# Kernel tuning notes

Measured on AMD Instinct MI355X. Metric: run time of the kernel, lower is better.

Reference implementation:

```python
import jax, jax.numpy as jnp
import numpy as np

B, S, I, H, HI = 1024, 64, 2048, 2048, 2048  # batch, num_high_states, input_dim, hidden_dim, high_dim
L = 4          # num recurrent layers
NH = 16        # num heads
HD = H // NH   # head dim
MAX_STEPS = 100


def setup_inputs() -> dict:
    key = jax.random.key(0)
    ks = iter(jax.random.split(key, 40))
    std = 0.02
    d = {}
    d["x"] = jax.random.normal(next(ks), (B, I), jnp.float32)
    d["high_state"] = jax.random.normal(next(ks), (B, HI), jnp.float32)
    d["high_states_history"] = jax.random.normal(next(ks), (B, S, HI), jnp.float32)
    d["hidden"] = jax.random.normal(next(ks), (L, B, H), jnp.float32) * 0.1
    # input projection + timestep embedding
    d["W_in"] = jax.random.normal(next(ks), (I, H), jnp.float32) * std
    d["b_in"] = jnp.zeros((H,), jnp.float32)
    d["ts_emb"] = jax.random.normal(next(ks), (MAX_STEPS, H), jnp.float32) * std
    # hierarchical attention projections
    d["Wq"] = jax.random.normal(next(ks), (H, H), jnp.float32) * std
    d["bq"] = jnp.zeros((H,), jnp.float32)
    d["Wk"] = jax.random.normal(next(ks), (HI, H), jnp.float32) * std
    d["bk"] = jnp.zeros((H,), jnp.float32)
    d["Wv"] = jax.random.normal(next(ks), (HI, H), jnp.float32) * std
    d["bv"] = jnp.zeros((H,), jnp.float32)
    d["Wo"] = jax.random.normal(next(ks), (H, H), jnp.float32) * std
    d["bo"] = jnp.zeros((H,), jnp.float32)
    # per-layer GRU-like gates, stacked over layers; Linear in = I+H = 2H
    for nm in ("Wu", "Wr", "Ws", "Wc"):
        d[nm] = jax.random.normal(next(ks), (L, 2 * H, H), jnp.float32) * std
    for nm in ("bu", "br", "bs", "bc"):
        d[nm] = jnp.zeros((L, H), jnp.float32)
    # layer norm
    d["ln_g"] = jnp.ones((H,), jnp.float32)
    d["ln_b"] = jnp.zeros((H,), jnp.float32)
    d["timestep"] = 5
    return d


def _forward(x, high_states_history, hidden, W_in, b_in, ts_emb,
             Wq, bq, Wk, bk, Wv, bv, Wo, bo,
             Wu, bu, Wr, br, Ws, bs, Wc, bc, ln_g, ln_b, timestep):
    # input projection + timestep encoding
    x = x @ W_in + b_in + ts_emb[timestep]  # [B,H]
    # hierarchical attention (single query per batch element)
    q = (x @ Wq + bq).reshape(B, NH, HD)
    k = (high_states_history @ Wk + bk).reshape(B, S, NH, HD)
    v = (high_states_history @ Wv + bv).reshape(B, S, NH, HD)
    scores = jnp.einsum("bhd,bshd->bhs", q, k) / np.sqrt(HD).astype(np.float32)
    attn = jax.nn.softmax(scores, axis=-1)  # [B,NH,S]
    ctx = jnp.einsum("bhs,bshd->bhd", attn, v).reshape(B, H)
    x = x + (ctx @ Wo + bo)
    # stacked GRU-like recurrent layers (loop over fixed small L)
    new_hidden = []
    for i in range(L):
        h = hidden[i]
        comb = jnp.concatenate([x, h], axis=1)  # [B,2H]
        u = jax.nn.sigmoid(comb @ Wu[i] + bu[i])
        r = jax.nn.sigmoid(comb @ Wr[i] + br[i])
        s = jax.nn.sigmoid(comb @ Ws[i] + bs[i])
        comb_r = jnp.concatenate([x, r * h], axis=1)
        cand = jax.nn.gelu(comb_r @ Wc[i] + bc[i], approximate=False)
        new_h = (1 - u) * h + u * (s * cand + (1 - s) * h)
        new_hidden.append(new_h)
        x = new_h  # dropout is identity in eval
    # layer norm (eps matches torch default 1e-5)
    mu = jnp.mean(x, axis=-1, keepdims=True)
    var = jnp.mean(jnp.square(x - mu), axis=-1, keepdims=True)
    out = (x - mu) * jax.lax.rsqrt(var + 1e-5) * ln_g + ln_b
    return out, jnp.stack(new_hidden)


def reference(x, high_state, high_states_history, hidden, W_in, b_in, ts_emb,
              Wq, bq, Wk, bk, Wv, bv, Wo, bo,
              Wu, bu, Wr, br, Ws, bs, Wc, bc, ln_g, ln_b, timestep):
    # high_state is accepted by the original signature but unused in the body
    return _forward(x, high_states_history, hidden, W_in, b_in, ts_emb,
                    Wq, bq, Wk, bk, Wv, bv, Wo, bo,
                    Wu, bu, Wr, br, Ws, bs, Wc, bc, ln_g, ln_b, timestep)
```

## Files before the change

kernel.cpp:

```cpp
#include <hip/hip_runtime.h>
#include <hip/hip_bf16.h>
#include <math.h>

#define B_  1024
#define S_  64
#define H_  2048
#define L_  4
#define NH_ 16
#define HD_ 128
#define WSLAB_ ((size_t)2048 * 4096)

typedef __attribute__((ext_vector_type(4))) float floatx4;
typedef __attribute__((ext_vector_type(8))) short shortx8;

__device__ __forceinline__ unsigned short f2bf(float f) {
  union { float f; unsigned int u; } v; v.f = f;
  unsigned int u = v.u;
  return (unsigned short)((u + 0x7fffu + ((u >> 16) & 1u)) >> 16);
}

__device__ __forceinline__ void gload16(const void* g, void* l) {
  __builtin_amdgcn_global_load_lds(
      (const __attribute__((address_space(1))) void*)g,
      (__attribute__((address_space(3))) void*)l, 16, 0, 0);
}

__global__ __launch_bounds__(256) void cvt_bf(
    const float* __restrict__ in, unsigned short* __restrict__ out, int n8)
{
  int i = blockIdx.x * 256 + threadIdx.x;
  if (i >= n8) return;
  const float4* p = (const float4*)in;
  float4 a = p[i * 2], b = p[i * 2 + 1];
  unsigned short o[8] = { f2bf(a.x), f2bf(a.y), f2bf(a.z), f2bf(a.w),
                          f2bf(b.x), f2bf(b.y), f2bf(b.z), f2bf(b.w) };
  ((uint4*)out)[i] = *(uint4*)o;
}

__global__ __launch_bounds__(256) void tconv4(
    const float* __restrict__ s0, const float* __restrict__ s1,
    const float* __restrict__ s2, const float* __restrict__ s3,
    unsigned short* __restrict__ dst, int K)
{
  const float* src = (blockIdx.z == 0) ? s0 : (blockIdx.z == 1) ? s1
                   : (blockIdx.z == 2) ? s2 : s3;
  unsigned short* out = dst + (size_t)blockIdx.z * 2048 * K;
  __shared__ float tile[64][65];
  int k0 = blockIdx.x * 64, n0 = blockIdx.y * 64;
  int t = threadIdx.x;
  int tr = t >> 4, tc = (t & 15) * 4;
  #pragma unroll
  for (int rep = 0; rep < 4; ++rep) {
    int kk = tr + rep * 16;
    float4 v = *(const float4*)(src + (size_t)(k0 + kk) * 2048 + n0 + tc);
    tile[kk][tc] = v.x; tile[kk][tc + 1] = v.y;
    tile[kk][tc + 2] = v.z; tile[kk][tc + 3] = v.w;
  }
  __syncthreads();
  int nr = t >> 2, kc = (t & 3) * 16;
  unsigned short o[16];
  #pragma unroll
  for (int j = 0; j < 16; ++j) o[j] = f2bf(tile[kc + j][nr]);
  *(uint4*)(out + (size_t)(n0 + nr) * K + k0 + kc)     = *(uint4*)&o[0];
  *(uint4*)(out + (size_t)(n0 + nr) * K + k0 + kc + 8) = *(uint4*)&o[8];
}

enum { EPI_XIN = 0, EPI_QB = 1, EPI_X2 = 2 };

template<int EPI, int MF, int NZ>
__global__ __launch_bounds__(256) void gemm128(
    int K,
    const unsigned short* __restrict__ A0,
    const unsigned short* __restrict__ BT,
    const float* __restrict__ b0,
    const float* __restrict__ tse, const int* __restrict__ tsp,
    const float* __restrict__ res,
    float* __restrict__ Cf, unsigned short* __restrict__ Cb)
{
  constexpr int BM = MF * 32;
  constexpr int NPAN = 16 * NZ;
  const int t = threadIdx.x, wid = t >> 6, lane = t & 63, lr = lane & 15, lg = lane >> 4;
  const int wr = wid >> 1, wc = wid & 1;
  const int g = blockIdx.x;
  const int m_base = (g / NPAN) * BM;
  const int pan = g % NPAN;
  const int n_base = (pan & 15) * 128;
  __shared__ unsigned short lds_a[BM * 32];
  __shared__ unsigned short lds_b[128 * 32];
  floatx4 acc[MF][4] = {};
  const int nkt = K >> 5;
  for (int kt = 0; kt < nkt; ++kt) {
    #pragma unroll
    for (int is = 0; is < BM / 64; ++is) {
      int idx = is * 256 + t;
      int row = idx >> 2, kc = idx & 3;
      int kcs = kc ^ ((row >> 1) & 3);
      int gk = kt * 32 + kcs * 8;
      gload16(A0 + (size_t)(m_base + row) * K + gk, &lds_a[(is * 256 + wid * 64) * 8]);
    }
    #pragma unroll
    for (int is = 0; is < 2; ++is) {
      int idx = is * 256 + t;
      int row = idx >> 2, kc = idx & 3;
      int kcs = kc ^ ((row >> 1) & 3);
      int gk = kt * 32 + kcs * 8;
      gload16(BT + (size_t)(n_base + row) * K + gk, &lds_b[(is * 256 + wid * 64) * 8]);
    }
    __syncthreads();
    const int sl = lg ^ ((lr >> 1) & 3);
    shortx8 af[MF], bfv[4];
    #pragma unroll
    for (int mt = 0; mt < MF; ++mt)
      af[mt] = *(shortx8*)&lds_a[(wr * (MF * 16) + mt * 16 + lr) * 32 + sl * 8];
    #pragma unroll
    for (int nt = 0; nt < 4; ++nt)
      bfv[nt] = *(shortx8*)&lds_b[(wc * 64 + nt * 16 + lr) * 32 + sl * 8];
    #pragma unroll
    for (int mt = 0; mt < MF; ++mt)
      #pragma unroll
      for (int nt = 0; nt < 4; ++nt)
        acc[mt][nt] = __builtin_amdgcn_mfma_f32_16x16x32_bf16(af[mt], bfv[nt], acc[mt][nt], 0, 0, 0);
    __syncthreads();
  }
  int ts = 0;
  if (EPI == EPI_XIN) ts = tsp[0];
  #pragma unroll
  for (int mt = 0; mt < MF; ++mt)
  #pragma unroll
  for (int nt = 0; nt < 4; ++nt)
  #pragma unroll
  for (int j = 0; j < 4; ++j) {
    int row = m_base + wr * (MF * 16) + mt * 16 + lg * 4 + j;
    int col = n_base + wc * 64 + nt * 16 + lr;
    size_t idx = (size_t)row * 2048 + col;
    float v = acc[mt][nt][j] + b0[col];
    if (EPI == EPI_XIN) {
      v += tse[(size_t)ts * 2048 + col];
      Cf[idx] = v; Cb[idx] = f2bf(v);
    } else if (EPI == EPI_QB) {
      Cb[idx] = f2bf(v);
    } else {
      v += res[idx]; Cb[idx] = f2bf(v);
    }
  }
}

__global__ __launch_bounds__(256, 4) void gemm_gates(
    const unsigned short* __restrict__ Ax, const unsigned short* __restrict__ Ah,
    const unsigned short* __restrict__ TW,
    const float* __restrict__ bu, const float* __restrict__ br, const float* __restrict__ bs,
    const float* __restrict__ Hf,
    float* __restrict__ U, float* __restrict__ Sg,
    unsigned short* __restrict__ rh, float* __restrict__ Cc)
{
  const int t = threadIdx.x, wid = t >> 6, lane = t & 63, lr = lane & 15, lg = lane >> 4;
  const int wr = wid >> 1, wc = wid & 1;
  const int g = blockIdx.x;
  const int m_base = (g >> 6) * 64;
  const int pan = g & 63;
  const int n_base = (pan & 15) * 128;
  const int z = pan >> 4;
  const unsigned short* BTz = TW + (size_t)z * WSLAB_;
  __shared__ unsigned short lds_a[64 * 32];
  __shared__ unsigned short lds_b[128 * 32];
  floatx4 acc[2][4] = {};
  const int nkt = (z == 3) ? 64 : 128;
  const int arow = t >> 2, akc = t & 3;
  const int akcs = akc ^ ((arow >> 1) & 3);
  for (int kt = 0; kt < nkt; ++kt) {
    {
      int gk = kt * 32 + akcs * 8;
      const unsigned short* ga;
      if (z == 3)           ga = Ax + (size_t)(m_base + arow) * 2048 + gk;
      else if (gk < 2048)   ga = Ax + (size_t)(m_base + arow) * 2048 + gk;
      else                  ga = Ah + (size_t)(m_base + arow) * 2048 + (gk - 2048);
      gload16(ga, &lds_a[wid * 512]);
    }
    #pragma unroll
    for (int is = 0; is < 2; ++is) {
      int idx = is * 256 + t;
      int row = idx >> 2, kc = idx & 3;
      int kcs = kc ^ ((row >> 1) & 3);
      int gk = kt * 32 + kcs * 8;
      gload16(BTz + (size_t)(n_base + row) * 4096 + gk, &lds_b[(is * 256 + wid * 64) * 8]);
    }
    __syncthreads();
    const int sl = lg ^ ((lr >> 1) & 3);
    shortx8 af[2], bfv[4];
    #pragma unroll
    for (int mt = 0; mt < 2; ++mt)
      af[mt] = *(shortx8*)&lds_a[(wr * 32 + mt * 16 + lr) * 32 + sl * 8];
    #pragma unroll
    for (int nt = 0; nt < 4; ++nt)
      bfv[nt] = *(shortx8*)&lds_b[(wc * 64 + nt * 16 + lr) * 32 + sl * 8];
    #pragma unroll
    for (int mt = 0; mt < 2; ++mt)
      #pragma unroll
      for (int nt = 0; nt < 4; ++nt)
        acc[mt][nt] = __builtin_amdgcn_mfma_f32_16x16x32_bf16(af[mt], bfv[nt], acc[mt][nt], 0, 0, 0);
    __syncthreads();
  }
  #pragma unroll
  for (int mt = 0; mt < 2; ++mt)
  #pragma unroll
  for (int nt = 0; nt < 4; ++nt)
  #pragma unroll
  for (int j = 0; j < 4; ++j) {
    int row = m_base + wr * 32 + mt * 16 + lg * 4 + j;
    int col = n_base + wc * 64 + nt * 16 + lr;
    size_t idx = (size_t)row * 2048 + col;
    float v = acc[mt][nt][j];
    if (z == 0)      U[idx]  = 1.f / (1.f + expf(-(v + bu[col])));
    else if (z == 1) rh[idx] = f2bf((1.f / (1.f + expf(-(v + br[col])))) * Hf[idx]);
    else if (z == 2) Sg[idx] = 1.f / (1.f + expf(-(v + bs[col])));
    else             Cc[idx] = v;
  }
}

__global__ __launch_bounds__(256, 4) void gemm_cand(
    const unsigned short* __restrict__ Arh, const unsigned short* __restrict__ TW,
    const float* __restrict__ bc, const float* __restrict__ Cc,
    const float* __restrict__ U, const float* __restrict__ Sg,
    const float* __restrict__ Hf,
    float* __restrict__ nh_f, unsigned short* __restrict__ nh_b)
{
  const int t = threadIdx.x, wid = t >> 6, lane = t & 63, lr = lane & 15, lg = lane >> 4;
  const int wr = wid >> 1, wc = wid & 1;
  const int g = blockIdx.x;
  const int m_base = (g >> 4) * 64;
  const int n_base = (g & 15) * 128;
  const unsigned short* BTz = TW + (size_t)3 * WSLAB_;
  __shared__ unsigned short lds_a[64 * 32];
  __shared__ unsigned short lds_b[128 * 32];
  floatx4 acc[2][4] = {};
  const int arow = t >> 2, akc = t & 3;
  const int akcs = akc ^ ((arow >> 1) & 3);
  for (int kt = 0; kt < 64; ++kt) {
    gload16(Arh + (size_t)(m_base + arow) * 2048 + kt * 32 + akcs * 8, &lds_a[wid * 512]);
    #pragma unroll
    for (int is = 0; is < 2; ++is) {
      int idx = is * 256 + t;
      int row = idx >> 2, kc = idx & 3;
      int kcs = kc ^ ((row >> 1) & 3);
      int gk = kt * 32 + kcs * 8;
      gload16(BTz + (size_t)(n_base + row) * 4096 + 2048 + gk, &lds_b[(is * 256 + wid * 64) * 8]);
    }
    __syncthreads();
    const int sl = lg ^ ((lr >> 1) & 3);
    shortx8 af[2], bfv[4];
    #pragma unroll
    for (int mt = 0; mt < 2; ++mt)
      af[mt] = *(shortx8*)&lds_a[(wr * 32 + mt * 16 + lr) * 32 + sl * 8];
    #pragma unroll
    for (int nt = 0; nt < 4; ++nt)
      bfv[nt] = *(shortx8*)&lds_b[(wc * 64 + nt * 16 + lr) * 32 + sl * 8];
    #pragma unroll
    for (int mt = 0; mt < 2; ++mt)
      #pragma unroll
      for (int nt = 0; nt < 4; ++nt)
        acc[mt][nt] = __builtin_amdgcn_mfma_f32_16x16x32_bf16(af[mt], bfv[nt], acc[mt][nt], 0, 0, 0);
    __syncthreads();
  }
  #pragma unroll
  for (int mt = 0; mt < 2; ++mt)
  #pragma unroll
  for (int nt = 0; nt < 4; ++nt)
  #pragma unroll
  for (int j = 0; j < 4; ++j) {
    int row = m_base + wr * 32 + mt * 16 + lg * 4 + j;
    int col = n_base + wc * 64 + nt * 16 + lr;
    size_t idx = (size_t)row * 2048 + col;
    float v = acc[mt][nt][j] + Cc[idx] + bc[col];
    float gl = 0.5f * v * (1.f + erff(v * 0.70710678118654752f));
    float u = U[idx], s = Sg[idx], hh = Hf[idx];
    float nh = (1.f - u) * hh + u * (s * gl + (1.f - s) * hh);
    nh_f[idx] = nh; nh_b[idx] = f2bf(nh);
  }
}

__global__ __launch_bounds__(256) void gemm_t(
    const unsigned short* __restrict__ Q, const unsigned short* __restrict__ Wk,
    unsigned short* __restrict__ T)
{
  const int t = threadIdx.x, wid = t >> 6, lane = t & 63, lr = lane & 15, lg = lane >> 4;
  const int wr = wid >> 1, wc = wid & 1;
  const int h = blockIdx.z, m_base = blockIdx.x * 64, n_base = blockIdx.y * 128;
  __shared__ unsigned short lds_a[64 * 32], lds_b[128 * 32];
  floatx4 acc[2][4] = {};
  const int arow = t >> 2, akc = t & 3;
  const int akcs = akc ^ ((arow >> 1) & 3);
  for (int kt = 0; kt < 4; ++kt) {
    gload16(Q + (size_t)(m_base + arow) * 2048 + h * 128 + kt * 32 + akcs * 8,
            &lds_a[wid * 512]);
    #pragma unroll
    for (int is = 0; is < 2; ++is) {
      int idx = is * 256 + t;
      int row = idx >> 2, kc = idx & 3;
      int kcs = kc ^ ((row >> 1) & 3);
      gload16(Wk + (size_t)(n_base + row) * 2048 + h * 128 + kt * 32 + kcs * 8,
              &lds_b[(is * 256 + wid * 64) * 8]);
    }
    __syncthreads();
    const int sl = lg ^ ((lr >> 1) & 3);
    shortx8 af[2], bfv[4];
    #pragma unroll
    for (int mt = 0; mt < 2; ++mt)
      af[mt] = *(shortx8*)&lds_a[(wr * 32 + mt * 16 + lr) * 32 + sl * 8];
    #pragma unroll
    for (int nt = 0; nt < 4; ++nt)
      bfv[nt] = *(shortx8*)&lds_b[(wc * 64 + nt * 16 + lr) * 32 + sl * 8];
    #pragma unroll
    for (int mt = 0; mt < 2; ++mt)
      #pragma unroll
      for (int nt = 0; nt < 4; ++nt)
        acc[mt][nt] = __builtin_amdgcn_mfma_f32_16x16x32_bf16(af[mt], bfv[nt], acc[mt][nt], 0, 0, 0);
    __syncthreads();
  }
  #pragma unroll
  for (int mt = 0; mt < 2; ++mt)
  #pragma unroll
  for (int nt = 0; nt < 4; ++nt)
  #pragma unroll
  for (int j = 0; j < 4; ++j) {
    int row_o = m_base + wr * 32 + mt * 16 + lg * 4 + j;
    int col   = n_base + wc * 64 + nt * 16 + lr;
    T[((size_t)row_o * 16 + h) * 2048 + col] = f2bf(acc[mt][nt][j]);
  }
}

__global__ __launch_bounds__(256) void attn_fused(
    const unsigned short* __restrict__ T, const float* __restrict__ hist,
    unsigned short* __restrict__ Wb)
{
  const int t = threadIdx.x;
  const int wid = t >> 6, lane = t & 63, lr = lane & 15, lg = lane >> 4;
  const int b = blockIdx.x;
  __shared__ unsigned short lds_t[16 * 72];
  __shared__ unsigned short lds_h[64 * 72];
  __shared__ float sc[16 * 68];
  __shared__ float ps[64 * 16];
  floatx4 acc = {};
  for (int kt = 0; kt < 32; ++kt) {
    { int row = t >> 4, c4 = t & 15;
      int k = kt * 64 + c4 * 4;
      ushort4 v = *(const ushort4*)(T + ((size_t)b * 16 + row) * 2048 + k);
      *(ushort4*)&lds_t[row * 72 + c4 * 4] = v; }
    #pragma unroll
    for (int rep = 0; rep < 4; ++rep) {
      int idx = t + rep * 256;
      int srow = idx >> 4, c4 = idx & 15;
      int k = kt * 64 + c4 * 4;
      float4 hv = *(const float4*)(hist + ((size_t)b * 64 + srow) * 2048 + k);
      ushort4 uv; uv.x = f2bf(hv.x); uv.y = f2bf(hv.y); uv.z = f2bf(hv.z); uv.w = f2bf(hv.w);
      *(ushort4*)&lds_h[srow * 72 + c4 * 4] = uv;
    }
    __syncthreads();
    #pragma unroll
    for (int ks = 0; ks < 2; ++ks) {
      shortx8 af = *(shortx8*)&lds_t[lr * 72 + ks * 32 + lg * 8];
      shortx8 bv = *(shortx8*)&lds_h[(wid * 16 + lr) * 72 + ks * 32 + lg * 8];
      acc = __builtin_amdgcn_mfma_f32_16x16x32_bf16(af, bv, acc, 0, 0, 0);
    }
    __syncthreads();
  }
  #pragma unroll
  for (int j = 0; j < 4; ++j)
    sc[(lg * 4 + j) * 68 + wid * 16 + lr] = acc[j] * 0.088388347648318447f;
  __syncthreads();
  if (t < 64) {
    int h = t >> 2, qd = t & 3;
    float vv[16];
    float m = -1e30f;
    #pragma unroll
    for (int zz = 0; zz < 16; ++zz) { vv[zz] = sc[h * 68 + qd * 16 + zz]; m = fmaxf(m, vv[zz]); }
    m = fmaxf(m, __shfl_xor(m, 1)); m = fmaxf(m, __shfl_xor(m, 2));
    float sum = 0.f;
    #pragma unroll
    for (int zz = 0; zz < 16; ++zz) { vv[zz] = expf(vv[zz] - m); sum += vv[zz]; }
    sum += __shfl_xor(sum, 1); sum += __shfl_xor(sum, 2);
    float inv = 1.f / sum;
    #pragma unroll
    for (int zz = 0; zz < 16; ++zz)
      ps[(qd * 16 + zz) * 16 + h] = vv[zz] * inv;
  }
  __syncthreads();
  const int i0 = t * 8;
  floatx4 wacc[16][2] = {};
  const floatx4* ps4 = (const floatx4*)ps;
  for (int s = 0; s < 64; ++s) {
    const float* hp = hist + ((size_t)b * 64 + s) * 2048 + i0;
    float4 h4a = *(const float4*)hp;
    float4 h4b = *(const float4*)(hp + 4);
    floatx4 hva = { h4a.x, h4a.y, h4a.z, h4a.w };
    floatx4 hvb = { h4b.x, h4b.y, h4b.z, h4b.w };
    #pragma unroll
    for (int hq = 0; hq < 4; ++hq) {
      floatx4 p = ps4[s * 4 + hq];
      wacc[hq * 4 + 0][0] += p.x * hva; wacc[hq * 4 + 0][1] += p.x * hvb;
      wacc[hq * 4 + 1][0] += p.y * hva; wacc[hq * 4 + 1][1] += p.y * hvb;
      wacc[hq * 4 + 2][0] += p.z * hva; wacc[hq * 4 + 2][1] += p.z * hvb;
      wacc[hq * 4 + 3][0] += p.w * hva; wacc[hq * 4 + 3][1] += p.w * hvb;
    }
  }
  #pragma unroll
  for (int h = 0; h < 16; ++h) {
    unsigned short o[8];
    #pragma unroll
    for (int j = 0; j < 4; ++j) { o[j] = f2bf(wacc[h][0][j]); o[4 + j] = f2bf(wacc[h][1][j]); }
    *(uint4*)(Wb + ((size_t)b * 16 + h) * 2048 + i0) = *(uint4*)o;
  }
}

__global__ __launch_bounds__(256) void gemm_ctx(
    const unsigned short* __restrict__ Wb, const unsigned short* __restrict__ WvT,
    const float* __restrict__ bv, unsigned short* __restrict__ ctx)
{
  const int t = threadIdx.x, wid = t >> 6, lane = t & 63, lr = lane & 15, lg = lane >> 4;
  const int wr = wid >> 1, wc = wid & 1;
  const int h = blockIdx.z, m_base = blockIdx.x * 64;
  __shared__ unsigned short lds_a[64 * 32], lds_b[128 * 32];
  floatx4 acc[2][4] = {};
  const int row = t >> 2, kc = t & 3;
  const int kcs = kc ^ ((row >> 1) & 3);
  for (int kt = 0; kt < 64; ++kt) {
    int gk = kt * 32 + kcs * 8;
    gload16(Wb  + ((size_t)(m_base + row) * 16 + h) * 2048 + gk, &lds_a[wid * 512]);
    gload16(WvT + (size_t)(h * 128 + row) * 2048 + gk,           &lds_b[wid * 512]);
    gload16(WvT + (size_t)(h * 128 + 64 + row) * 2048 + gk,      &lds_b[2048 + wid * 512]);
    __syncthreads();
    const int sl = lg ^ ((lr >> 1) & 3);
    shortx8 af[2], bfv[4];
    #pragma unroll
    for (int mt = 0; mt < 2; ++mt)
      af[mt] = *(shortx8*)&lds_a[(wr * 32 + mt * 16 + lr) * 32 + sl * 8];
    #pragma unroll
    for (int nt = 0; nt < 4; ++nt)
      bfv[nt] = *(shortx8*)&lds_b[(wc * 64 + nt * 16 + lr) * 32 + sl * 8];
    #pragma unroll
    for (int mt = 0; mt < 2; ++mt)
      #pragma unroll
      for (int nt = 0; nt < 4; ++nt)
        acc[mt][nt] = __builtin_amdgcn_mfma_f32_16x16x32_bf16(af[mt], bfv[nt], acc[mt][nt], 0, 0, 0);
    __syncthreads();
  }
  #pragma unroll
  for (int mt = 0; mt < 2; ++mt)
  #pragma unroll
  for (int nt = 0; nt < 4; ++nt)
  #pragma unroll
  for (int j = 0; j < 4; ++j) {
    int row_o = m_base + wr * 32 + mt * 16 + lg * 4 + j;
    int cl = wc * 64 + nt * 16 + lr;
    int gcol = h * 128 + cl;
    ctx[(size_t)row_o * 2048 + gcol] = f2bf(acc[mt][nt][j] + bv[gcol]);
  }
}

__global__ __launch_bounds__(256) void lnorm(
    const float* __restrict__ X, const float* __restrict__ gma,
    const float* __restrict__ bta, float* __restrict__ out)
{
  const int row = blockIdx.x, t = threadIdx.x;
  float4 a = *(const float4*)(X + (size_t)row * 2048 + t * 4);
  float4 c = *(const float4*)(X + (size_t)row * 2048 + 1024 + t * 4);
  float sum = a.x + a.y + a.z + a.w + c.x + c.y + c.z + c.w;
  float sq = a.x*a.x + a.y*a.y + a.z*a.z + a.w*a.w + c.x*c.x + c.y*c.y + c.z*c.z + c.w*c.w;
  #pragma unroll
  for (int off = 1; off < 64; off <<= 1) {
    sum += __shfl_xor(sum, off);
    sq  += __shfl_xor(sq, off);
  }
  __shared__ float red[8];
  int wid = t >> 6, lane = t & 63;
  if (lane == 0) { red[wid] = sum; red[wid + 4] = sq; }
  __syncthreads();
  sum = red[0] + red[1] + red[2] + red[3];
  sq  = red[4] + red[5] + red[6] + red[7];
  float mu = sum * (1.f / 2048.f);
  float var = sq * (1.f / 2048.f) - mu * mu;
  float rs = rsqrtf(var + 1e-5f);
  const float* pa = &a.x; const float* pc = &c.x;
  #pragma unroll
  for (int j = 0; j < 4; ++j) {
    int col = t * 4 + j;
    out[(size_t)row * 2048 + col] = (pa[j] - mu) * rs * gma[col] + bta[col];
  }
  #pragma unroll
  for (int j = 0; j < 4; ++j) {
    int col = 1024 + t * 4 + j;
    out[(size_t)row * 2048 + col] = (pc[j] - mu) * rs * gma[col] + bta[col];
  }
}

extern "C" void kernel_launch(void* const* d_in, const int* in_sizes, int n_in,
                              void* d_out, int out_size, void* d_ws, size_t ws_size,
                              hipStream_t stream) {
  (void)in_sizes; (void)n_in; (void)out_size; (void)ws_size;
  const float* x      = (const float*)d_in[0];
  const float* hist   = (const float*)d_in[2];
  const float* hidden = (const float*)d_in[3];
  const float* W_in   = (const float*)d_in[4];
  const float* b_in   = (const float*)d_in[5];
  const float* ts_emb = (const float*)d_in[6];
  const float* Wq     = (const float*)d_in[7];
  const float* bq     = (const float*)d_in[8];
  const float* Wk     = (const float*)d_in[9];
  const float* Wv     = (const float*)d_in[11];
  const float* bv     = (const float*)d_in[12];
  const float* Wo     = (const float*)d_in[13];
  const float* bo     = (const float*)d_in[14];
  const float* Wu     = (const float*)d_in[15];
  const float* Wr     = (const float*)d_in[16];
  const float* Wsg    = (const float*)d_in[17];
  const float* Wc     = (const float*)d_in[18];
  const float* bu     = (const float*)d_in[19];
  const float* br     = (const float*)d_in[20];
  const float* bs     = (const float*)d_in[21];
  const float* bc     = (const float*)d_in[22];
  const float* ln_g   = (const float*)d_in[23];
  const float* ln_b   = (const float*)d_in[24];
  const int*   tsp    = (const int*)d_in[25];
  float* out = (float*)d_out;

  const size_t BH = (size_t)B_ * H_;
  char* w = (char*)d_ws;
  auto take = [&](size_t bytes) { char* p = w; w += bytes; return p; };

  unsigned short* TW   = (unsigned short*)take((size_t)4 * WSLAB_ * 2);
  unsigned short* Tb   = (unsigned short*)take((size_t)B_ * 16 * 2048 * 2);
  unsigned short* WT4  = (unsigned short*)take((size_t)4 * H_ * H_ * 2);
  unsigned short* WinT = WT4;
  unsigned short* WqT  = WT4 + (size_t)H_ * H_;
  unsigned short* WvT  = WT4 + (size_t)2 * H_ * H_;
  unsigned short* WoT  = WT4 + (size_t)3 * H_ * H_;
  unsigned short* Wkb  = (unsigned short*)take((size_t)H_ * H_ * 2);
  unsigned short* x_bf   = (unsigned short*)take(BH * 2);
  unsigned short* h_bf   = (unsigned short*)take((size_t)L_ * BH * 2);
  unsigned short* xin_bf = (unsigned short*)take(BH * 2);
  unsigned short* q_bf   = (unsigned short*)take(BH * 2);
  unsigned short* ctx_bf = (unsigned short*)take(BH * 2);
  unsigned short* x2_bf  = (unsigned short*)take(BH * 2);
  unsigned short* rh_bf  = (unsigned short*)take(BH * 2);
  unsigned short* xa     = (unsigned short*)take(BH * 2);
  unsigned short* xb     = (unsigned short*)take(BH * 2);
  float* U   = (float*)take(BH * 4);
  float* Sg  = (float*)take(BH * 4);
  float* Cc  = (float*)take(BH * 4);
  float* XIN = out;

  dim3 blk(256);

  cvt_bf<<<dim3(1024), blk, 0, stream>>>(x, x_bf, (int)(BH / 8));
  cvt_bf<<<dim3(4096), blk, 0, stream>>>(hidden, h_bf, (int)(L_ * BH / 8));
  cvt_bf<<<dim3(2048), blk, 0, stream>>>(Wk, Wkb, (int)((size_t)H_ * H_ / 8));
  tconv4<<<dim3(32, 32, 4), blk, 0, stream>>>(W_in, Wq, Wv, Wo, WT4, 2048);

  gemm128<EPI_XIN, 2, 1><<<dim3(256), blk, 0, stream>>>(
      2048, x_bf, WinT, b_in, ts_emb, tsp, nullptr, XIN, xin_bf);
  gemm128<EPI_QB, 2, 1><<<dim3(256), blk, 0, stream>>>(
      2048, xin_bf, WqT, bq, nullptr, nullptr, nullptr, nullptr, q_bf);
  gemm_t<<<dim3(16, 16, 16), blk, 0, stream>>>(q_bf, Wkb, Tb);
  attn_fused<<<dim3(1024), blk, 0, stream>>>(Tb, hist, Tb);
  gemm_ctx<<<dim3(16, 1, 16), blk, 0, stream>>>(Tb, WvT, bv, ctx_bf);
  gemm128<EPI_X2, 2, 1><<<dim3(256), blk, 0, stream>>>(
      2048, ctx_bf, WoT, bo, nullptr, nullptr, XIN, nullptr, x2_bf);

  unsigned short* xcur = x2_bf;
  for (int i = 0; i < L_; ++i) {
    const float* h_i = hidden + (size_t)i * BH;
    float* nh_f = out + BH + (size_t)i * BH;
    unsigned short* nh_b = (i & 1) ? xb : xa;
    tconv4<<<dim3(64, 32, 4), blk, 0, stream>>>(
        Wu + (size_t)i * WSLAB_, Wr + (size_t)i * WSLAB_,
        Wsg + (size_t)i * WSLAB_, Wc + (size_t)i * WSLAB_, TW, 4096);
    gemm_gates<<<dim3(1024), blk, 0, stream>>>(
        xcur, h_bf + (size_t)i * BH, TW,
        bu + (size_t)i * H_, br + (size_t)i * H_, bs + (size_t)i * H_,
        h_i, U, Sg, rh_bf, Cc);
    gemm_cand<<<dim3(256), blk, 0, stream>>>(
        rh_bf, TW, bc + (size_t)i * H_, Cc, U, Sg, h_i, nh_f, nh_b);
    xcur = nh_b;
  }

  lnorm<<<dim3(1024), blk, 0, stream>>>(out + BH + (size_t)3 * BH, ln_g, ln_b, out);
}
```

Baseline: 1.262 ms.

## Overlap next-layer weight transpose with candidate GEMM via double-buffered slabs

Merges the next layer's fp32-to-bf16 weight transpose into the candidate GEMM launch as extra blocks. Two weight slabs are used as a double buffer so the conversion for layer i+1 runs alongside the 256-block cand GEMM for layer i, which on its own underfills the GPU. Layer 0's slab is converted up front. The cost is an extra 64MB workspace buffer and no longer forcing launch_bounds occupancy 4 on the GEMM blocks, which may change register allocation.

After: 1.250 ms. No clear change (-1.0%).

```diff
diff --git a/kernel.cpp b/kernel.cpp
--- a/kernel.cpp
+++ b/kernel.cpp
@@ -217,64 +217,96 @@
   }
 }
 
-__global__ __launch_bounds__(256, 4) void gemm_cand(
+__global__ __launch_bounds__(256) void cand_tconv(
     const unsigned short* __restrict__ Arh, const unsigned short* __restrict__ TW,
     const float* __restrict__ bc, const float* __restrict__ Cc,
     const float* __restrict__ U, const float* __restrict__ Sg,
     const float* __restrict__ Hf,
-    float* __restrict__ nh_f, unsigned short* __restrict__ nh_b)
-{
-  const int t = threadIdx.x, wid = t >> 6, lane = t & 63, lr = lane & 15, lg = lane >> 4;
-  const int wr = wid >> 1, wc = wid & 1;
-  const int g = blockIdx.x;
-  const int m_base = (g >> 4) * 64;
-  const int n_base = (g & 15) * 128;
-  const unsigned short* BTz = TW + (size_t)3 * WSLAB_;
-  __shared__ unsigned short lds_a[64 * 32];
-  __shared__ unsigned short lds_b[128 * 32];
-  floatx4 acc[2][4] = {};
-  const int arow = t >> 2, akc = t & 3;
-  const int akcs = akc ^ ((arow >> 1) & 3);
-  for (int kt = 0; kt < 64; ++kt) {
-    gload16(Arh + (size_t)(m_base + arow) * 2048 + kt * 32 + akcs * 8, &lds_a[wid * 512]);
-    #pragma unroll
-    for (int is = 0; is < 2; ++is) {
-      int idx = is * 256 + t;
-      int row = idx >> 2, kc = idx & 3;
-      int kcs = kc ^ ((row >> 1) & 3);
-      int gk = kt * 32 + kcs * 8;
-      gload16(BTz + (size_t)(n_base + row) * 4096 + 2048 + gk, &lds_b[(is * 256 + wid * 64) * 8]);
-    }
-    __syncthreads();
-    const int sl = lg ^ ((lr >> 1) & 3);
-    shortx8 af[2], bfv[4];
+    float* __restrict__ nh_f, unsigned short* __restrict__ nh_b,
+    const float* __restrict__ Wun, const float* __restrict__ Wrn,
+    const float* __restrict__ Wsn, const float* __restrict__ Wcn,
+    unsigned short* __restrict__ TWnext)
+{
+  __shared__ __align__(16) float smem[4224];
+  const int t = threadIdx.x;
+  if (blockIdx.x < 256) {
+    unsigned short* lds_a = (unsigned short*)smem;
+    unsigned short* lds_b = (unsigned short*)smem + 2048;
+    const int wid = t >> 6, lane = t & 63, lr = lane & 15, lg = lane >> 4;
+    const int wr = wid >> 1, wc = wid & 1;
+    const int g = blockIdx.x;
+    const int m_base = (g >> 4) * 64;
+    const int n_base = (g & 15) * 128;
+    const unsigned short* BTz = TW + (size_t)3 * WSLAB_;
+    floatx4 acc[2][4] = {};
+    const int arow = t >> 2, akc = t & 3;
+    const int akcs = akc ^ ((arow >> 1) & 3);
+    for (int kt = 0; kt < 64; ++kt) {
+      gload16(Arh + (size_t)(m_base + arow) * 2048 + kt * 32 + akcs * 8, &lds_a[wid * 512]);
+      #pragma unroll
+      for (int is = 0; is < 2; ++is) {
+        int idx = is * 256 + t;
+        int row = idx >> 2, kc = idx & 3;
+        int kcs = kc ^ ((row >> 1) & 3);
+        int gk = kt * 32 + kcs * 8;
+        gload16(BTz + (size_t)(n_base + row) * 4096 + 2048 + gk, &lds_b[(is * 256 + wid * 64) * 8]);
+      }
+      __syncthreads();
+      const int sl = lg ^ ((lr >> 1) & 3);
+      shortx8 af[2], bfv[4];
+      #pragma unroll
+      for (int mt = 0; mt < 2; ++mt)
+        af[mt] = *(shortx8*)&lds_a[(wr * 32 + mt * 16 + lr) * 32 + sl * 8];
+      #pragma unroll
+      for (int nt = 0; nt < 4; ++nt)
+        bfv[nt] = *(shortx8*)&lds_b[(wc * 64 + nt * 16 + lr) * 32 + sl * 8];
+      #pragma unroll
+      for (int mt = 0; mt < 2; ++mt)
+        #pragma unroll
+        for (int nt = 0; nt < 4; ++nt)
+          acc[mt][nt] = __builtin_amdgcn_mfma_f32_16x16x32_bf16(af[mt], bfv[nt], acc[mt][nt], 0, 0, 0);
+      __syncthreads();
+    }
     #pragma unroll
     for (int mt = 0; mt < 2; ++mt)
-      af[mt] = *(shortx8*)&lds_a[(wr * 32 + mt * 16 + lr) * 32 + sl * 8];
     #pragma unroll
     for (int nt = 0; nt < 4; ++nt)
-      bfv[nt] = *(shortx8*)&lds_b[(wc * 64 + nt * 16 + lr) * 32 + sl * 8];
-    #pragma unroll
-    for (int mt = 0; mt < 2; ++mt)
-      #pragma unroll
-      for (int nt = 0; nt < 4; ++nt)
-        acc[mt][nt] = __builtin_amdgcn_mfma_f32_16x16x32_bf16(af[mt], bfv[nt], acc[mt][nt], 0, 0, 0);
-    __syncthreads();
-  }
-  #pragma unroll
-  for (int mt = 0; mt < 2; ++mt)
-  #pragma unroll
-  for (int nt = 0; nt < 4; ++nt)
-  #pragma unroll
-  for (int j = 0; j < 4; ++j) {
-    int row = m_base + wr * 32 + mt * 16 + lg * 4 + j;
-    int col = n_base + wc * 64 + nt * 16 + lr;
-    size_t idx = (size_t)row * 2048 + col;
-    float v = acc[mt][nt][j] + Cc[idx] + bc[col];
-    float gl = 0.5f * v * (1.f + erff(v * 0.70710678118654752f));
-    float u = U[idx], s = Sg[idx], hh = Hf[idx];
-    float nh = (1.f - u) * hh + u * (s * gl + (1.f - s) * hh);
-    nh_f[idx] = nh; nh_b[idx] = f2bf(nh);
+    #pragma unroll
+    for (int j = 0; j < 4; ++j) {
+      int row = m_base + wr * 32 + mt * 16 + lg * 4 + j;
+      int col = n_base + wc * 64 + nt * 16 + lr;
+      size_t idx = (size_t)row * 2048 + col;
+      float v = acc[mt][nt][j] + Cc[idx] + bc[col];
+      float gl = 0.5f * v * (1.f + erff(v * 0.70710678118654752f));
+      float u = U[idx], s = Sg[idx], hh = Hf[idx];
+      float nh = (1.f - u) * hh + u * (s * gl + (1.f - s) * hh);
+      nh_f[idx] = nh; nh_b[idx] = f2bf(nh);
+    }
+  } else {
+    if (TWnext == nullptr) return;
+    float (*tile)[65] = (float(*)[65])smem;
+    int bid = blockIdx.x - 256;
+    int z = bid >> 11;
+    int rem = bid & 2047;
+    int k0 = (rem >> 5) * 64;
+    int n0 = (rem & 31) * 64;
+    const float* src = (z == 0) ? Wun : (z == 1) ? Wrn : (z == 2) ? Wsn : Wcn;
+    unsigned short* outp = TWnext + (size_t)z * WSLAB_;
+    int tr = t >> 4, tc = (t & 15) * 4;
+    #pragma unroll
+    for (int rep = 0; rep < 4; ++rep) {
+      int kk = tr + rep * 16;
+      float4 v = *(const float4*)(src + (size_t)(k0 + kk) * 2048 + n0 + tc);
+      tile[kk][tc] = v.x; tile[kk][tc + 1] = v.y;
+      tile[kk][tc + 2] = v.z; tile[kk][tc + 3] = v.w;
+    }
+    __syncthreads();
+    int nr = t >> 2, kc = (t & 3) * 16;
+    unsigned short o[16];
+    #pragma unroll
+    for (int j = 0; j < 16; ++j) o[j] = f2bf(tile[kc + j][nr]);
+    *(uint4*)(outp + (size_t)(n0 + nr) * 4096 + k0 + kc)     = *(uint4*)&o[0];
+    *(uint4*)(outp + (size_t)(n0 + nr) * 4096 + k0 + kc + 8) = *(uint4*)&o[8];
   }
 }
 
@@ -526,7 +558,8 @@
   char* w = (char*)d_ws;
   auto take = [&](size_t bytes) { char* p = w; w += bytes; return p; };
 
-  unsigned short* TW   = (unsigned short*)take((size_t)4 * WSLAB_ * 2);
+  unsigned short* TW0  = (unsigned short*)take((size_t)4 * WSLAB_ * 2);
+  unsigned short* TW1  = (unsigned short*)take((size_t)4 * WSLAB_ * 2);
   unsigned short* Tb   = (unsigned short*)take((size_t)B_ * 16 * 2048 * 2);
   unsigned short* WT4  = (unsigned short*)take((size_t)4 * H_ * H_ * 2);
   unsigned short* WinT = WT4;
@@ -554,6 +587,7 @@
   cvt_bf<<<dim3(4096), blk, 0, stream>>>(hidden, h_bf, (int)(L_ * BH / 8));
   cvt_bf<<<dim3(2048), blk, 0, stream>>>(Wk, Wkb, (int)((size_t)H_ * H_ / 8));
   tconv4<<<dim3(32, 32, 4), blk, 0, stream>>>(W_in, Wq, Wv, Wo, WT4, 2048);
+  tconv4<<<dim3(64, 32, 4), blk, 0, stream>>>(Wu, Wr, Wsg, Wc, TW0, 4096);
 
   gemm128<EPI_XIN, 2, 1><<<dim3(256), blk, 0, stream>>>(
       2048, x_bf, WinT, b_in, ts_emb, tsp, nullptr, XIN, xin_bf);
@@ -570,15 +604,17 @@
     const float* h_i = hidden + (size_t)i * BH;
     float* nh_f = out + BH + (size_t)i * BH;
     unsigned short* nh_b = (i & 1) ? xb : xa;
-    tconv4<<<dim3(64, 32, 4), blk, 0, stream>>>(
-        Wu + (size_t)i * WSLAB_, Wr + (size_t)i * WSLAB_,
-        Wsg + (size_t)i * WSLAB_, Wc + (size_t)i * WSLAB_, TW, 4096);
+    unsigned short* TWcur = (i & 1) ? TW1 : TW0;
+    unsigned short* TWnxt = (i < 3) ? ((i & 1) ? TW0 : TW1) : nullptr;
     gemm_gates<<<dim3(1024), blk, 0, stream>>>(
-        xcur, h_bf + (size_t)i * BH, TW,
+        xcur, h_bf + (size_t)i * BH, TWcur,
         bu + (size_t)i * H_, br + (size_t)i * H_, bs + (size_t)i * H_,
         h_i, U, Sg, rh_bf, Cc);
-    gemm_cand<<<dim3(256), blk, 0, stream>>>(
-        rh_bf, TW, bc + (size_t)i * H_, Cc, U, Sg, h_i, nh_f, nh_b);
+    int grid = (i < 3) ? 8448 : 256;
+    size_t off = (size_t)(i + 1) * WSLAB_;
+    cand_tconv<<<dim3(grid), blk, 0, stream>>>(
+        rh_bf, TWcur, bc + (size_t)i * H_, Cc, U, Sg, h_i, nh_f, nh_b,
+        Wu + off, Wr + off, Wsg + off, Wc + off, TWnxt);
     xcur = nh_b;
   }
 
```
